# Kernel optimization log

Measured on AMD Instinct MI355X. Metric: run time of the kernel, lower is better.

## Reference

```python
import jax, jax.numpy as jnp
import numpy as np

def setup_inputs() -> dict:
    key = jax.random.key(0)
    k1, k2 = jax.random.split(key)
    B, T, C = 32, 1024, 384
    x = jax.random.normal(k1, (B, T, C), dtype=jnp.float32)
    duration = jax.random.randint(k2, (B, T), 0, 8, dtype=jnp.int64)
    return {"x": x, "duration": duration, "max_mel_len": 4096}


def reference(x, duration, max_mel_len):
    # Equivalent to the original per-batch expand-matrix matmul:
    # out[b, m] = x[b, t] where t is the token whose duration-interval covers
    # frame m; frames beyond sum(duration[b]) are zero.
    B, T, C = x.shape
    cs = jnp.cumsum(duration, axis=1)                      # [B, T] end offsets
    total = cs[:, -1]                                      # [B] expanded lengths
    frames = jnp.arange(max_mel_len)                       # [M]
    # token index for each output frame: first t with cs[b, t] > m
    tok = jax.vmap(lambda c: jnp.searchsorted(c, frames, side="right"))(cs)  # [B, M]
    tok = jnp.clip(tok, 0, T - 1)
    out = jnp.take_along_axis(x, tok[:, :, None], axis=1)  # [B, M, C]
    valid = frames[None, :] < total[:, None]               # [B, M]
    out = jnp.where(valid[:, :, None], out, jnp.zeros((), dtype=x.dtype))
    return out, total
```

## Files before the change

### kernel.cpp

```cpp
#include <hip/hip_runtime.h>
#include <stdint.h>

#define BB 32
#define TT 1024
#define CC 384
#define MAXMEL 4096

typedef float f4 __attribute__((ext_vector_type(4)));

__device__ __forceinline__ int block_scan_1024(const int* __restrict__ dur, int b,
                                               int* s_cs) {
    __shared__ int s_wsum[16];
    const int tid = threadIdx.x;
    const int lane = tid & 63;
    const int wid = tid >> 6;
    int v = dur[b * TT + tid];
    #pragma unroll
    for (int off = 1; off < 64; off <<= 1) {
        int n = __shfl_up(v, off, 64);
        if (lane >= off) v += n;
    }
    if (lane == 63) s_wsum[wid] = v;
    __syncthreads();
    if (wid == 0 && lane < 16) {
        int w = s_wsum[lane];
        #pragma unroll
        for (int off = 1; off < 16; off <<= 1) {
            int n = __shfl_up(w, off, 64);
            if (lane >= off) w += n;
        }
        s_wsum[lane] = w;
    }
    __syncthreads();
    if (wid > 0) v += s_wsum[wid - 1];
    s_cs[tid] = v;
    __syncthreads();
    return s_cs[TT - 1];
}


__global__ __launch_bounds__(1024) void lr_scan_tok16(const int* __restrict__ dur,
                                                      uint16_t* __restrict__ tok,
                                                      float* __restrict__ out_total) {
    __shared__ int s_cs[TT];
    const int b = blockIdx.y;
    const int tid = threadIdx.x;
    const int total = block_scan_1024(dur, b, s_cs);
    if (blockIdx.x == 0 && tid == 0) out_total[b] = (float)total;

    const int f = blockIdx.x * 1024 + tid;
    uint16_t t = 0xFFFFu;
    if (f < total) {
        int lo = 0, hi = TT;
        while (lo < hi) {
            int mid = (lo + hi) >> 1;
            if (s_cs[mid] <= f) lo = mid + 1; else hi = mid;
        }
        t = (uint16_t)min(lo, TT - 1);
    }
    tok[b * MAXMEL + f] = t;
}

__global__ __launch_bounds__(512) void lr_expand_tok16(const float* __restrict__ x,
                                                       const uint16_t* __restrict__ tok,
                                                       float* __restrict__ out) {
    const int b = blockIdx.y;
    const int frame = blockIdx.x * 16 + (threadIdx.x >> 5);
    const int lane = threadIdx.x & 31;
    const uint32_t t = tok[b * MAXMEL + frame];
    f4* outp = (f4*)(out + ((size_t)b * MAXMEL + frame) * CC);
    if (t != 0xFFFFu) {
        const f4* src = (const f4*)(x + ((size_t)b * TT + t) * CC);
        #pragma unroll
        for (int k = 0; k < 3; ++k) {
            f4 v = src[lane + k * 32];
            __builtin_nontemporal_store(v, &outp[lane + k * 32]);
        }
    } else {
        const f4 z = {0.f, 0.f, 0.f, 0.f};
        #pragma unroll
        for (int k = 0; k < 3; ++k) __builtin_nontemporal_store(z, &outp[lane + k * 32]);
    }
}


__global__ __launch_bounds__(1024) void lr_scan_cs(const int* __restrict__ dur,
                                                   int* __restrict__ cs,
                                                   float* __restrict__ out_total) {
    __shared__ int s_cs[TT];
    const int b = blockIdx.x;
    const int tid = threadIdx.x;
    const int total = block_scan_1024(dur, b, s_cs);
    cs[b * TT + tid] = s_cs[tid];
    if (tid == 0) out_total[b] = (float)total;
}

__global__ __launch_bounds__(1024) void lr_expand_search(const float* __restrict__ x,
                                                         const int* __restrict__ cs,
                                                         float* __restrict__ out) {
    __shared__ int s_cs[TT];
    const int b = blockIdx.y;
    const int tid = threadIdx.x;
    s_cs[tid] = cs[b * TT + tid];
    __syncthreads();
    const int total = s_cs[TT - 1];
    const int frame = blockIdx.x * 64 + (tid >> 4);
    const int lane = tid & 15;
    f4* outp = (f4*)(out + ((size_t)b * MAXMEL + frame) * CC);
    if (frame < total) {
        int lo = 0, hi = TT;
        while (lo < hi) {
            int mid = (lo + hi) >> 1;
            if (s_cs[mid] <= frame) lo = mid + 1; else hi = mid;
        }
        const int t = min(lo, TT - 1);
        const f4* src = (const f4*)(x + ((size_t)b * TT + t) * CC);
        #pragma unroll
        for (int k = 0; k < 6; ++k) outp[lane + k * 16] = src[lane + k * 16];
    } else {
        const f4 z = {0.f, 0.f, 0.f, 0.f};
        #pragma unroll
        for (int k = 0; k < 6; ++k) outp[lane + k * 16] = z;
    }
}

extern "C" void kernel_launch(void* const* d_in, const int* in_sizes, int n_in,
                              void* d_out, int out_size, void* d_ws, size_t ws_size,
                              hipStream_t stream) {
    const float* x = (const float*)d_in[0];
    const int* dur = (const int*)d_in[1];
    float* out = (float*)d_out;
    float* out_total = out + (size_t)BB * MAXMEL * CC;

    if (ws_size >= (size_t)BB * MAXMEL * sizeof(uint16_t)) {
        uint16_t* tok = (uint16_t*)d_ws;
        lr_scan_tok16<<<dim3(4, BB), 1024, 0, stream>>>(dur, tok, out_total);
        lr_expand_tok16<<<dim3(MAXMEL / 16, BB), 512, 0, stream>>>(x, tok, out);
    } else {
        int* cs = (int*)d_ws;
        lr_scan_cs<<<BB, 1024, 0, stream>>>(dur, cs, out_total);
        lr_expand_search<<<dim3(MAXMEL / 64, BB), 1024, 0, stream>>>(x, cs, out);
    }
}
```

Before: 239.3 us.

## Fuse duration scan and frame expansion into a single kernel

Replaces the separate scan-to-token kernel and expand kernel with one kernel. Each block recomputes the per-batch cumulative sum in shared memory, then does a branchless binary search for 128 frames and copies rows with nontemporal stores. This removes one launch and the token-index round trip through global memory. In exchange, the scan is recomputed redundantly by every block in a batch.

Result: slower. 244.4 us (+2.1%).

```diff
diff --git a/kernel.cpp b/kernel.cpp
--- a/kernel.cpp
+++ b/kernel.cpp
@@ -5,6 +5,7 @@
 #define TT 1024
 #define CC 384
 #define MAXMEL 4096
+#define FPB 128
 
 typedef float f4 __attribute__((ext_vector_type(4)));
 
@@ -38,89 +39,42 @@
     return s_cs[TT - 1];
 }
 
-
-__global__ __launch_bounds__(1024) void lr_scan_tok16(const int* __restrict__ dur,
-                                                      uint16_t* __restrict__ tok,
-                                                      float* __restrict__ out_total) {
+__global__ __launch_bounds__(1024) void lr_fused(const float* __restrict__ x,
+                                                 const int* __restrict__ dur,
+                                                 float* __restrict__ out,
+                                                 float* __restrict__ out_total) {
     __shared__ int s_cs[TT];
     const int b = blockIdx.y;
     const int tid = threadIdx.x;
     const int total = block_scan_1024(dur, b, s_cs);
     if (blockIdx.x == 0 && tid == 0) out_total[b] = (float)total;
 
-    const int f = blockIdx.x * 1024 + tid;
-    uint16_t t = 0xFFFFu;
-    if (f < total) {
-        int lo = 0, hi = TT;
-        while (lo < hi) {
-            int mid = (lo + hi) >> 1;
-            if (s_cs[mid] <= f) lo = mid + 1; else hi = mid;
+    const int lane = tid & 31;
+    const int f0 = blockIdx.x * FPB + (tid >> 5);
+    const float* __restrict__ xb = x + (size_t)b * TT * CC;
+    float* __restrict__ ob = out + (size_t)b * MAXMEL * CC;
+
+    #pragma unroll
+    for (int j = 0; j < FPB / 32; ++j) {
+        const int frame = f0 + j * 32;
+        f4* outp = (f4*)(ob + (size_t)frame * CC);
+        if (frame < total) {
+            int pos = 0;
+            #pragma unroll
+            for (int s = 512; s >= 1; s >>= 1) {
+                if (s_cs[pos + s - 1] <= frame) pos += s;
+            }
+            const int t = min(pos, TT - 1);
+            const f4* src = (const f4*)(xb + (size_t)t * CC);
+            #pragma unroll
+            for (int k = 0; k < 3; ++k)
+                __builtin_nontemporal_store(src[lane + k * 32], &outp[lane + k * 32]);
+        } else {
+            const f4 z = {0.f, 0.f, 0.f, 0.f};
+            #pragma unroll
+            for (int k = 0; k < 3; ++k)
+                __builtin_nontemporal_store(z, &outp[lane + k * 32]);
         }
-        t = (uint16_t)min(lo, TT - 1);
-    }
-    tok[b * MAXMEL + f] = t;
-}
-
-__global__ __launch_bounds__(512) void lr_expand_tok16(const float* __restrict__ x,
-                                                       const uint16_t* __restrict__ tok,
-                                                       float* __restrict__ out) {
-    const int b = blockIdx.y;
-    const int frame = blockIdx.x * 16 + (threadIdx.x >> 5);
-    const int lane = threadIdx.x & 31;
-    const uint32_t t = tok[b * MAXMEL + frame];
-    f4* outp = (f4*)(out + ((size_t)b * MAXMEL + frame) * CC);
-    if (t != 0xFFFFu) {
-        const f4* src = (const f4*)(x + ((size_t)b * TT + t) * CC);
-        #pragma unroll
-        for (int k = 0; k < 3; ++k) {
-            f4 v = src[lane + k * 32];
-            __builtin_nontemporal_store(v, &outp[lane + k * 32]);
-        }
-    } else {
-        const f4 z = {0.f, 0.f, 0.f, 0.f};
-        #pragma unroll
-        for (int k = 0; k < 3; ++k) __builtin_nontemporal_store(z, &outp[lane + k * 32]);
-    }
-}
-
-
-__global__ __launch_bounds__(1024) void lr_scan_cs(const int* __restrict__ dur,
-                                                   int* __restrict__ cs,
-                                                   float* __restrict__ out_total) {
-    __shared__ int s_cs[TT];
-    const int b = blockIdx.x;
-    const int tid = threadIdx.x;
-    const int total = block_scan_1024(dur, b, s_cs);
-    cs[b * TT + tid] = s_cs[tid];
-    if (tid == 0) out_total[b] = (float)total;
-}
-
-__global__ __launch_bounds__(1024) void lr_expand_search(const float* __restrict__ x,
-                                                         const int* __restrict__ cs,
-                                                         float* __restrict__ out) {
-    __shared__ int s_cs[TT];
-    const int b = blockIdx.y;
-    const int tid = threadIdx.x;
-    s_cs[tid] = cs[b * TT + tid];
-    __syncthreads();
-    const int total = s_cs[TT - 1];
-    const int frame = blockIdx.x * 64 + (tid >> 4);
-    const int lane = tid & 15;
-    f4* outp = (f4*)(out + ((size_t)b * MAXMEL + frame) * CC);
-    if (frame < total) {
-        int lo = 0, hi = TT;
-        while (lo < hi) {
-            int mid = (lo + hi) >> 1;
-            if (s_cs[mid] <= frame) lo = mid + 1; else hi = mid;
-        }
-        const int t = min(lo, TT - 1);
-        const f4* src = (const f4*)(x + ((size_t)b * TT + t) * CC);
-        #pragma unroll
-        for (int k = 0; k < 6; ++k) outp[lane + k * 16] = src[lane + k * 16];
-    } else {
-        const f4 z = {0.f, 0.f, 0.f, 0.f};
-        #pragma unroll
-        for (int k = 0; k < 6; ++k) outp[lane + k * 16] = z;
     }
 }
 
@@ -132,13 +86,5 @@
     float* out = (float*)d_out;
     float* out_total = out + (size_t)BB * MAXMEL * CC;
 
-    if (ws_size >= (size_t)BB * MAXMEL * sizeof(uint16_t)) {
-        uint16_t* tok = (uint16_t*)d_ws;
-        lr_scan_tok16<<<dim3(4, BB), 1024, 0, stream>>>(dur, tok, out_total);
-        lr_expand_tok16<<<dim3(MAXMEL / 16, BB), 512, 0, stream>>>(x, tok, out);
-    } else {
-        int* cs = (int*)d_ws;
-        lr_scan_cs<<<BB, 1024, 0, stream>>>(dur, cs, out_total);
-        lr_expand_search<<<dim3(MAXMEL / 64, BB), 1024, 0, stream>>>(x, cs, out);
-    }
+    lr_fused<<<dim3(MAXMEL / FPB, BB), 1024, 0, stream>>>(x, dur, out, out_total);
 }
```
